# Performance work log

Measured on AMD Instinct MI355X. Metric: run time of the kernel, lower is better.

## Reference

```python
import jax, jax.numpy as jnp
import numpy as np

B, T, D, H, F, Q = 256, 512, 64, 1024, 8, 3

def setup_inputs() -> dict:
    key = jax.random.key(0)
    ks = jax.random.split(key, 6)
    scale = 0.05
    x  = jax.random.normal(ks[0], (B, T, D), dtype=jnp.float32)
    Wx = jax.random.normal(ks[1], (D, 4 * H), dtype=jnp.float32) * scale  # input->gates (no bias, flax dense_i)
    Wh = jax.random.normal(ks[2], (H, 4 * H), dtype=jnp.float32) * scale  # hidden->gates
    b  = jnp.zeros((4 * H,), dtype=jnp.float32)                           # bias on hidden path (flax dense_h)
    Wr = jax.random.normal(ks[3], (F, H, Q), dtype=jnp.float32) * scale   # per-feature Dense(H -> 1*Q)
    br = jnp.zeros((F, Q), dtype=jnp.float32)
    return {"x": x, "Wx": Wx, "Wh": Wh, "b": b, "Wr": Wr, "br": br}

def _lstm_last_hidden(x, Wx, Wh, b):
    # x: (B, T, D) -> scan over time, return final hidden (B, H)
    Bn = x.shape[0]
    h0 = jnp.zeros((Bn, H), dtype=x.dtype)
    c0 = jnp.zeros((Bn, H), dtype=x.dtype)
    # precompute input projection for all timesteps: (T, B, 4H)
    xz = jnp.einsum('btd,dk->tbk', x, Wx)
    def step(carry, xz_t):
        h, c = carry
        z = xz_t + h @ Wh + b                      # (B, 4H)
        i, f, g, o = jnp.split(z, 4, axis=-1)      # flax gate order: i, f, g, o
        i = jax.nn.sigmoid(i)
        f = jax.nn.sigmoid(f)
        g = jnp.tanh(g)
        o = jax.nn.sigmoid(o)
        c_new = f * c + i * g
        h_new = o * jnp.tanh(c_new)
        return (h_new, c_new), None
    (h_fin, c_fin), _ = jax.lax.scan(step, (h0, c0), xz)
    return h_fin

def reference(x, Wx, Wh, b, Wr, br):
    h_last = _lstm_last_hidden(x, Wx, Wh, b)            # (B, H)
    # per-feature small Dense heads, stacked: (B, F, Q)
    out = jnp.einsum('bh,fhq->bfq', h_last, Wr) + br
    return out.astype(jnp.float32)
```

## Files before the change

kernel.cpp:

```cpp
#include <hip/hip_runtime.h>
#include <hip/hip_bf16.h>

#define B_   256
#define T_   512
#define D_   64
#define H_   1024
#define NG   4096
#define KTOT 1088
#define WPAD 1096

typedef __attribute__((ext_vector_type(8)))  short short8;
typedef __attribute__((ext_vector_type(4)))  float f32x4;
typedef __attribute__((ext_vector_type(16))) float f32x16;

static __device__ __forceinline__ float tanh_clamped(float u) {
  u = fminf(fmaxf(u, -15.0f), 15.0f);
  float e = __expf(-2.0f * u);
  return (1.0f - e) / (1.0f + e);
}
static __device__ __forceinline__ unsigned short f2bf(float f) {
  union { float f; unsigned int u; } v; v.f = f;
  unsigned int r = (v.u + 0x7FFFu + ((v.u >> 16) & 1u)) >> 16;
  return (unsigned short)r;
}

template <int CTRL>
static __device__ __forceinline__ float qperm(float v) {
  union { float f; int i; } a, b;
  a.f = v;
  b.i = __builtin_amdgcn_update_dpp(0, a.i, CTRL, 0xF, 0xF, true);
  return b.f;
}

__global__ void k_zero_flags(int* flags) {
  int gid = blockIdx.x * 256 + threadIdx.x;
  if (gid < 4096) flags[gid] = 0;
}

__global__ void k_pack_w(const float* __restrict__ Wx, const float* __restrict__ Wh,
                         unsigned short* __restrict__ Wp) {
  __shared__ float tile[64][65];
  int nt = blockIdx.x & 63;
  int kt = blockIdx.x >> 6;
  int tx = threadIdx.x & 63, ty = threadIdx.x >> 6;
#pragma unroll
  for (int i = 0; i < 16; ++i) {
    int kl = i * 4 + ty;
    int k  = kt * 64 + kl;
    int n  = nt * 64 + tx;
    int oc = ((n & 3) << 10) | (n >> 2);
    float v = (k < D_) ? Wx[k * NG + oc] : Wh[(k - D_) * NG + oc];
    tile[kl][tx] = v;
  }
  __syncthreads();
#pragma unroll
  for (int i = 0; i < 16; ++i) {
    int nl = i * 4 + ty;
    int kl = tx;
    Wp[(size_t)(nt * 64 + nl) * KTOT + kt * 64 + kl] = f2bf(tile[kl][nl]);
  }
}

__global__ void k_pack_x(const float* __restrict__ x, unsigned short* __restrict__ xbt) {
  int gid = blockIdx.x * 256 + threadIdx.x;
  int b  = gid & 255;
  int kk = (gid >> 8) & 7;
  int t  = gid >> 11;
  const float* src = x + ((size_t)b * T_ + t) * 64 + kk * 8;
  short8 v;
#pragma unroll
  for (int i = 0; i < 8; ++i) v[i] = (short)f2bf(src[i]);
  *(short8*)(xbt + (size_t)gid * 8) = v;
}

__launch_bounds__(256, 1)
__global__ void k_scan(const unsigned short* __restrict__ Wp,
                       const unsigned short* __restrict__ xbt,
                       unsigned short* __restrict__ hbt,
                       float* __restrict__ hf,
                       const float* __restrict__ bias,
                       int* __restrict__ flags) {
  __shared__ unsigned short Wl[64 * WPAD];
  __shared__ float exch[4][16][64];
  __shared__ unsigned short hstage[4][32][8];
  __shared__ int blkcnt;
  const int tid  = threadIdx.x;
  const int bid  = blockIdx.x;
  const int m    = (bid >> 1) & 3;
  const int nt   = ((bid >> 3) << 1) | (bid & 1);
  const int n0   = nt * 64;
  const int wave = tid >> 6;
  const int lane = tid & 63;
  const int wr = wave >> 1, wc = wave & 1;

  if (tid == 0) blkcnt = 0;
  for (int i = tid; i < 64 * (KTOT / 8); i += 256) {
    int c  = i / (KTOT / 8);
    int kk = i - c * (KTOT / 8);
    short8 v = *(const short8*)(Wp + (size_t)(n0 + c) * KTOT + kk * 8);
    *(short8*)((char*)Wl + c * (WPAD * 2) + kk * 16) = v;
  }
  __syncthreads();

  const int khalf = lane >> 5;
  const int rowA  = m * 64 + wr * 32 + (lane & 31);
  const int colB  = wc * 32 + (lane & 31);
  const int n     = n0 + colB;
  const int oc    = ((n & 3) << 10) | (n >> 2);
  const float bv  = bias[oc];
  const int s     = lane & 3;
  const int q     = (lane & 31) >> 2;
  const int jH    = n >> 2;
  const char* WlK = (const char*)Wl + (size_t)(wc * 32 + (lane & 31)) * (WPAD * 2) + khalf * 16;
  const char* WlS = (const char*)Wl + (size_t)((1 - wc) * 32 + (lane & 31)) * (WPAD * 2) + khalf * 16;

  float c_state[16];
#pragma unroll
  for (int r = 0; r < 16; ++r) c_state[r] = 0.0f;

  int* myflag = flags + (m * 64 + nt) * 16;
  const int pidx = (lane < 32) ? (wc * 32 + lane) : nt;
  int* pollp  = flags + (m * 64 + pidx) * 16;

  const unsigned int voff0 = (unsigned)(khalf * 4096 + rowA * 16);
  const unsigned int vstore0 = (unsigned)(((nt * 2 + wc) * 256 + m * 64 + wr * 32) * 16);

  unsigned int vx[4];
#pragma unroll
  for (int f = 0; f < 4; ++f) vx[f] = (unsigned)((f * 2 + khalf) * 4096 + rowA * 16);

  short8 ax[4];
  {
    const unsigned short* xb = xbt;
#pragma unroll
    for (int f = 0; f < 4; ++f)
      asm volatile("global_load_dwordx4 %0, %1, %2"
                   : "=v"(ax[f]) : "v"(vx[f]), "s"(xb));
  }

  for (int t = 0; t < T_; ++t) {
    f32x16 accK;
#pragma unroll
    for (int r = 0; r < 16; ++r) accK[r] = bv;

    asm volatile("s_waitcnt vmcnt(0)" ::: "memory");
    __builtin_amdgcn_sched_barrier(0);
#pragma unroll
    for (int kt = 0; kt < 4; ++kt) {
      short8 b8 = *(const short8*)(WlK + kt * 32);
      accK = __builtin_amdgcn_mfma_f32_32x32x16_bf16(ax[kt], b8, accK, 0, 0, 0);
    }

    if (t > 0) {
      __builtin_amdgcn_sched_barrier(0);
      for (;;) {
        int v = __hip_atomic_load(pollp, __ATOMIC_RELAXED, __HIP_MEMORY_SCOPE_AGENT);
        if (__all(v >= t)) break;
      }
      const unsigned short* hsrc = hbt + (size_t)((t + 1) & 1) * 128 * 2048;

      short8 aH[32];
#pragma unroll
      for (int j = 0; j < 32; ++j) {
        unsigned int vo = voff0 + (unsigned)((wc * 32 + j) * 8192);
        asm volatile("global_load_dwordx4 %0, %1, %2 sc0 sc1"
                     : "=v"(aH[j]) : "v"(vo), "s"(hsrc));
      }
      f32x16 accS;
#pragma unroll
      for (int r = 0; r < 16; ++r) accS[r] = 0.0f;

#pragma unroll
      for (int g = 0; g < 4; ++g) {
        switch (g) {
          case 0: asm volatile("s_waitcnt vmcnt(24)" ::: "memory"); break;
          case 1: asm volatile("s_waitcnt vmcnt(16)" ::: "memory"); break;
          case 2: asm volatile("s_waitcnt vmcnt(8)"  ::: "memory"); break;
          case 3: asm volatile("s_waitcnt vmcnt(0)"  ::: "memory"); break;
        }
        __builtin_amdgcn_sched_barrier(0);
#pragma unroll
        for (int jj = 0; jj < 8; ++jj) {
          int j  = g * 8 + jj;
          int kt = wc * 32 + j;
          short8 bk = *(const short8*)(WlK + 128 + kt * 32);
          short8 bs = *(const short8*)(WlS + 128 + kt * 32);
          accK = __builtin_amdgcn_mfma_f32_32x32x16_bf16(aH[j], bk, accK, 0, 0, 0);
          accS = __builtin_amdgcn_mfma_f32_32x32x16_bf16(aH[j], bs, accS, 0, 0, 0);
        }
      }

#pragma unroll
      for (int r = 0; r < 16; ++r) exch[wave][r][lane] = accS[r];
      __syncthreads();
#pragma unroll
      for (int r = 0; r < 16; ++r) accK[r] += exch[wave ^ 1][r][lane];
      __syncthreads();
    }

#pragma unroll
    for (int r = 0; r < 16; ++r) {
      float z  = accK[r];
      float u  = (s == 2) ? z : 0.5f * z;
      float tv = tanh_clamped(u);
      float av = (s == 2) ? tv : 0.5f * (1.0f + tv);
      float x1 = qperm<0xB1>(av);
      float x2 = qperm<0x4E>(av);
      float x3 = qperm<0x1B>(av);
      float i_ = (s == 0) ? av : (s == 1) ? x1 : (s == 2) ? x2 : x3;
      float f_ = (s == 1) ? av : (s == 0) ? x1 : (s == 3) ? x2 : x3;
      float g_ = (s == 2) ? av : (s == 3) ? x1 : (s == 0) ? x2 : x3;
      float o_ = (s == 3) ? av : (s == 2) ? x1 : (s == 1) ? x2 : x3;
      float cn = f_ * c_state[r] + i_ * g_;
      c_state[r] = cn;
      float hn = o_ * tanh_clamped(cn);
      if (s == 0) {
        int rloc = 4 * khalf + (r & 3) + 8 * (r >> 2);
        if (t < T_ - 1) {
          hstage[wave][rloc][q] = f2bf(hn);
        } else {
          hf[(size_t)(m * 64 + wr * 32 + rloc) * H_ + jH] = hn;
        }
      }
    }

    if (t < T_ - 1) {
      asm volatile("s_waitcnt lgkmcnt(0)" ::: "memory");
      unsigned short* hdst = hbt + (size_t)(t & 1) * 128 * 2048;
      if (lane < 32) {
        f32x4 v = *(const f32x4*)&hstage[wave][lane][0];
        unsigned int vo = vstore0 + (unsigned)(lane * 16);
        asm volatile("global_store_dwordx4 %0, %1, %2 sc0 sc1"
                     :: "v"(vo), "v"(v), "s"(hdst) : "memory");
      }
      {
        const unsigned short* xb = xbt + (size_t)(t + 1) * 16384;
#pragma unroll
        for (int f = 0; f < 4; ++f)
          asm volatile("global_load_dwordx4 %0, %1, %2"
                       : "=v"(ax[f]) : "v"(vx[f]), "s"(xb));
      }
      asm volatile("s_waitcnt vmcnt(4)" ::: "memory");
      if (lane == 0) {
        int old = __hip_atomic_fetch_add(&blkcnt, 1, __ATOMIC_RELAXED,
                                         __HIP_MEMORY_SCOPE_WORKGROUP);
        if (old == 4 * t + 3) {
          unsigned int fv = (unsigned)(t + 1);
          asm volatile("global_store_dword %0, %1, %2 sc0 sc1"
                       :: "v"(0u), "v"(fv), "s"(myflag) : "memory");
        }
      }
    }
  }
}

__global__ void k_head(const float* __restrict__ hf, const float* __restrict__ Wr,
                       const float* __restrict__ br, float* __restrict__ out) {
  int bf = blockIdx.x;
  int b = bf >> 3, f = bf & 7;
  int lane = threadIdx.x;
  float s0 = 0.f, s1 = 0.f, s2 = 0.f;
  for (int j = lane; j < H_; j += 64) {
    float h = hf[(size_t)b * H_ + j];
    const float* w = Wr + ((size_t)f * H_ + j) * 3;
    s0 = fmaf(h, w[0], s0); s1 = fmaf(h, w[1], s1); s2 = fmaf(h, w[2], s2);
  }
#pragma unroll
  for (int o = 32; o >= 1; o >>= 1) {
    s0 += __shfl_xor(s0, o); s1 += __shfl_xor(s1, o); s2 += __shfl_xor(s2, o);
  }
  if (lane == 0) {
    out[bf * 3 + 0] = s0 + br[f * 3 + 0];
    out[bf * 3 + 1] = s1 + br[f * 3 + 1];
    out[bf * 3 + 2] = s2 + br[f * 3 + 2];
  }
}

extern "C" void kernel_launch(void* const* d_in, const int* in_sizes, int n_in,
                              void* d_out, int out_size, void* d_ws, size_t ws_size,
                              hipStream_t stream) {
  const float* x    = (const float*)d_in[0];
  const float* Wx   = (const float*)d_in[1];
  const float* Wh   = (const float*)d_in[2];
  const float* bias = (const float*)d_in[3];
  const float* Wr   = (const float*)d_in[4];
  const float* br   = (const float*)d_in[5];
  float* out = (float*)d_out;

  char* ws = (char*)d_ws;
  unsigned short* Wp  = (unsigned short*)ws;
  unsigned short* xbt = (unsigned short*)(ws + 8912896);
  unsigned short* hbt = (unsigned short*)(ws + 8912896 + 16777216);
  float* hf           = (float*)(ws + 8912896 + 16777216 + 1048576);
  int* flags          = (int*)(ws + 8912896 + 16777216 + 1048576 + 1048576);

  k_zero_flags<<<16, 256, 0, stream>>>(flags);
  k_pack_w<<<17 * 64, 256, 0, stream>>>(Wx, Wh, Wp);
  k_pack_x<<<4096, 256, 0, stream>>>(x, xbt);
  k_scan<<<256, 256, 0, stream>>>(Wp, xbt, hbt, hf, bias, flags);
  k_head<<<2048, 64, 0, stream>>>(hf, Wr, br, out);
}
```

Measured before the change: 3.664 ms.

## Replace block barriers with pairwise wave flags and per-row-half readiness flags

Swaps the two __syncthreads around the split-K partial-sum exchange for point-to-point sequence counters between each wave and its partner. Inter-block readiness now uses one flag per row half (wr) instead of one per block, so consumers of half the rows can start without waiting for the other half. The aim is to cut serialization on the recurrent critical path, at the cost of spin-waiting on LDS atomics and more complex ordering that depends on the memory model.

```diff
diff --git a/kernel.cpp b/kernel.cpp
--- a/kernel.cpp
+++ b/kernel.cpp
@@ -83,7 +83,9 @@
   __shared__ unsigned short Wl[64 * WPAD];
   __shared__ float exch[4][16][64];
   __shared__ unsigned short hstage[4][32][8];
-  __shared__ int blkcnt;
+  __shared__ int wseq[4];
+  __shared__ int rseq[4];
+  __shared__ int pcnt[2];
   const int tid  = threadIdx.x;
   const int bid  = blockIdx.x;
   const int m    = (bid >> 1) & 3;
@@ -93,7 +95,8 @@
   const int lane = tid & 63;
   const int wr = wave >> 1, wc = wave & 1;
 
-  if (tid == 0) blkcnt = 0;
+  if (tid < 4) { wseq[tid] = 0; rseq[tid] = 0; }
+  if (tid < 2) pcnt[tid] = 0;
   for (int i = tid; i < 64 * (KTOT / 8); i += 256) {
     int c  = i / (KTOT / 8);
     int kk = i - c * (KTOT / 8);
@@ -118,9 +121,9 @@
 #pragma unroll
   for (int r = 0; r < 16; ++r) c_state[r] = 0.0f;
 
-  int* myflag = flags + (m * 64 + nt) * 16;
-  const int pidx = (lane < 32) ? (wc * 32 + lane) : nt;
-  int* pollp  = flags + (m * 64 + pidx) * 16;
+  int* flagline = flags + (m * 64 + nt) * 16;
+  const unsigned int fo = (unsigned)(wr * 16);
+  int* pollp  = flags + (m * 64 + wc * 32 + (lane & 31)) * 16 + wr * 4;
 
   const unsigned int voff0 = (unsigned)(khalf * 4096 + rowA * 16);
   const unsigned int vstore0 = (unsigned)(((nt * 2 + wc) * 256 + m * 64 + wr * 32) * 16);
@@ -190,12 +193,24 @@
         }
       }
 
+      for (;;) {
+        int v = __hip_atomic_load(&rseq[wave ^ 1], __ATOMIC_RELAXED, __HIP_MEMORY_SCOPE_WORKGROUP);
+        if (v >= t - 1) break;
+      }
+      asm volatile("" ::: "memory");
 #pragma unroll
       for (int r = 0; r < 16; ++r) exch[wave][r][lane] = accS[r];
-      __syncthreads();
+      asm volatile("s_waitcnt lgkmcnt(0)" ::: "memory");
+      __hip_atomic_store(&wseq[wave], t, __ATOMIC_RELAXED, __HIP_MEMORY_SCOPE_WORKGROUP);
+      for (;;) {
+        int v = __hip_atomic_load(&wseq[wave ^ 1], __ATOMIC_RELAXED, __HIP_MEMORY_SCOPE_WORKGROUP);
+        if (v >= t) break;
+      }
+      asm volatile("" ::: "memory");
 #pragma unroll
       for (int r = 0; r < 16; ++r) accK[r] += exch[wave ^ 1][r][lane];
-      __syncthreads();
+      asm volatile("s_waitcnt lgkmcnt(0)" ::: "memory");
+      __hip_atomic_store(&rseq[wave], t, __ATOMIC_RELAXED, __HIP_MEMORY_SCOPE_WORKGROUP);
     }
 
 #pragma unroll
@@ -242,12 +257,12 @@
       }
       asm volatile("s_waitcnt vmcnt(4)" ::: "memory");
       if (lane == 0) {
-        int old = __hip_atomic_fetch_add(&blkcnt, 1, __ATOMIC_RELAXED,
+        int old = __hip_atomic_fetch_add(&pcnt[wr], 1, __ATOMIC_RELAXED,
                                          __HIP_MEMORY_SCOPE_WORKGROUP);
-        if (old == 4 * t + 3) {
+        if (old == 2 * t + 1) {
           unsigned int fv = (unsigned)(t + 1);
           asm volatile("global_store_dword %0, %1, %2 sc0 sc1"
-                       :: "v"(0u), "v"(fv), "s"(myflag) : "memory");
+                       :: "v"(fo), "v"(fv), "s"(flagline) : "memory");
         }
       }
     }
```

Measured after the change: 3.224 ms, median of 2. 12.0% less time.
